# Performance work log

Hardware: AMD Instinct MI355X
Metric: run time of the kernel (lower is better)

The kernel has to match this reference:

```python
import jax, jax.numpy as jnp
from jax import lax
import numpy as np

B, T, D, H, N_MID = 1024, 256, 64, 128, 1000000

def setup_inputs() -> dict:
    key = jax.random.key(0)
    ks = jax.random.split(key, 7)
    item_his = jax.random.randint(ks[0], (B, T), 0, N_MID)
    seq_lens = jax.random.randint(ks[1], (B,), 0, T)
    embedding = jax.random.normal(ks[2], (N_MID, D), dtype=jnp.float32) * 0.05
    gate_kernel = jax.random.normal(ks[3], (D + H, 2 * H), dtype=jnp.float32) * 0.05
    gate_bias = jax.random.normal(ks[4], (2 * H,), dtype=jnp.float32) * 0.05
    cand_kernel = jax.random.normal(ks[5], (D + H, H), dtype=jnp.float32) * 0.05
    cand_bias = jax.random.normal(ks[6], (H,), dtype=jnp.float32) * 0.05
    return {"item_his": item_his, "seq_lens": seq_lens, "embedding": embedding,
            "gate_kernel": gate_kernel, "gate_bias": gate_bias,
            "cand_kernel": cand_kernel, "cand_bias": cand_bias}

def _gru_final_state(x, seq_lens, gate_kernel, gate_bias, cand_kernel, cand_bias):
    # x: [B, T, D]; TF GRUCell math with dynamic_rnn sequence_length masking.
    b, t, d = x.shape
    h_dim = cand_bias.shape[0]
    mask = jnp.arange(t)[None, :] < seq_lens[:, None]  # [B, T]

    def step(h, inp):
        xt, m = inp  # xt: [B, D], m: [B]
        xh = jnp.concatenate([xt, h], axis=-1)              # [B, D+H]
        g = jax.nn.sigmoid(xh @ gate_kernel + gate_bias)    # [B, 2H]
        r, u = jnp.split(g, 2, axis=-1)
        xrh = jnp.concatenate([xt, r * h], axis=-1)
        c = jnp.tanh(xrh @ cand_kernel + cand_bias)
        h_new = u * h + (1.0 - u) * c
        h = jnp.where(m[:, None], h_new, h)  # copy-through past seq end
        return h, None

    h0 = jnp.zeros((b, h_dim), dtype=x.dtype)
    xs = (jnp.swapaxes(x, 0, 1), jnp.swapaxes(mask, 0, 1))
    hT, _ = lax.scan(step, h0, xs)
    return hT

def reference(item_his, seq_lens, embedding, gate_kernel, gate_bias, cand_kernel, cand_bias):
    x = embedding[item_his]  # [B, T, D]
    user_eb = _gru_final_state(x, seq_lens, gate_kernel, gate_bias, cand_kernel, cand_bias)
    return user_eb
```

## Files before the change

kernel.cpp:

```cpp
#include <hip/hip_runtime.h>


#define T_   256
#define D_   64
#define H_   128
#define SROW 208

typedef _Float16 half8_t  __attribute__((ext_vector_type(8)));
typedef float    floatx4  __attribute__((ext_vector_type(4)));

__global__ __launch_bounds__(512, 2) void gru_mfma(
    const int* __restrict__ item_his,
    const int* __restrict__ seq_lens,
    const float* __restrict__ emb,
    const float* __restrict__ Wg,
    const float* __restrict__ bg,
    const float* __restrict__ Wc,
    const float* __restrict__ bc,
    float* __restrict__ out)
{
    __shared__ __align__(16) _Float16 XA[16][SROW];
    __shared__ __align__(16) _Float16 XC[16][SROW];

    const int tid  = threadIdx.x;
    const int w    = tid >> 6;
    const int lane = tid & 63;
    const int row0 = blockIdx.x * 4;

    const int bq = lane >> 4;
    const int bn = lane & 15;
    half8_t BG0[6], BG1[6], BC6[6];
    #pragma unroll
    for (int kt = 0; kt < 6; ++kt) {
        half8_t f0, f1, fc;
        #pragma unroll
        for (int i = 0; i < 8; ++i) {
            const int k = kt * 32 + bq * 8 + i;
            f0[i] = (_Float16)Wg[k * 256 + (w * 16 + bn)];
            f1[i] = (_Float16)Wg[k * 256 + (128 + w * 16 + bn)];
            fc[i] = (_Float16)Wc[k * 128 + (w * 16 + bn)];
        }
        BG0[kt] = f0; BG1[kt] = f1; BC6[kt] = fc;
    }

    const float bgR = bg[w * 16 + bn];
    const float bgU = bg[128 + w * 16 + bn];
    const float bcC = bc[w * 16 + bn];

    int len[4];
    #pragma unroll
    for (int r = 0; r < 4; ++r) len[r] = seq_lens[row0 + r];
    const int maxlen = max(max(len[0], len[1]), max(len[2], len[3]));

    {
        unsigned* pa = (unsigned*)&XA[0][0];
        unsigned* pc = (unsigned*)&XC[0][0];
        for (int i = tid; i < 16 * SROW / 2; i += 512) { pa[i] = 0u; pc[i] = 0u; }
    }
    __syncthreads();

    const int  row_l = w >> 1;
    const int  d_l   = (w & 1) * 32 + (lane & 31);
    const bool ldr   = (lane < 32);

    float xprev = 0.f;
    if (ldr) {
        const int idx = item_his[(row0 + row_l) * T_ + 0];
        xprev = emb[(size_t)idx * D_ + d_l];
        const _Float16 xh = (_Float16)xprev;
        XA[row_l][d_l] = xh;
        XC[row_l][d_l] = xh;
    }
    float h[4] = {0.f, 0.f, 0.f, 0.f};
    float u[4] = {0.f, 0.f, 0.f, 0.f};
    __syncthreads();

    for (int t = 0; t < maxlen; ++t) {
        if (ldr) XC[row_l][d_l] = (_Float16)xprev;
        float xnew = 0.f;
        if (ldr) {
            const int idx = item_his[(row0 + row_l) * T_ + (t + 1)];
            xnew = emb[(size_t)idx * D_ + d_l];
        }

        floatx4 aR = {0.f, 0.f, 0.f, 0.f};
        floatx4 aU = {0.f, 0.f, 0.f, 0.f};
        #pragma unroll
        for (int kt = 0; kt < 6; ++kt) {
            const half8_t af = *(const half8_t*)&XA[lane & 15][kt * 32 + (lane >> 4) * 8];
            aR = __builtin_amdgcn_mfma_f32_16x16x32_f16(af, BG0[kt], aR, 0, 0, 0);
            aU = __builtin_amdgcn_mfma_f32_16x16x32_f16(af, BG1[kt], aU, 0, 0, 0);
        }
        if (lane < 16) {
            #pragma unroll
            for (int r = 0; r < 4; ++r) {
                const float rg = 1.f / (1.f + __expf(-(aR[r] + bgR)));
                u[r]           = 1.f / (1.f + __expf(-(aU[r] + bgU)));
                XC[r][64 + w * 16 + lane] = (_Float16)(rg * h[r]);
            }
        }
        __syncthreads();

        if (ldr) XA[row_l][d_l] = (_Float16)xnew;

        floatx4 aC = {0.f, 0.f, 0.f, 0.f};
        #pragma unroll
        for (int kt = 0; kt < 6; ++kt) {
            const half8_t af = *(const half8_t*)&XC[lane & 15][kt * 32 + (lane >> 4) * 8];
            aC = __builtin_amdgcn_mfma_f32_16x16x32_f16(af, BC6[kt], aC, 0, 0, 0);
        }
        if (lane < 16) {
            #pragma unroll
            for (int r = 0; r < 4; ++r) {
                float s = aC[r] + bcC;
                s = fminf(fmaxf(s, -15.f), 15.f);
                const float e = __expf(2.f * s);
                const float c = (e - 1.f) / (e + 1.f);
                const float hn = u[r] * h[r] + (1.f - u[r]) * c;
                if (t < len[r]) h[r] = hn;
                XA[r][64 + w * 16 + lane] = (_Float16)h[r];
            }
        }
        xprev = xnew;
        __syncthreads();
    }

    if (lane < 16) {
        #pragma unroll
        for (int r = 0; r < 4; ++r)
            out[(row0 + r) * H_ + w * 16 + lane] = h[r];
    }
}

extern "C" void kernel_launch(void* const* d_in, const int* in_sizes, int n_in,
                              void* d_out, int out_size, void* d_ws, size_t ws_size,
                              hipStream_t stream) {
    const int*   item_his = (const int*)d_in[0];
    const int*   seq_lens = (const int*)d_in[1];
    const float* emb      = (const float*)d_in[2];
    const float* Wg       = (const float*)d_in[3];
    const float* bg       = (const float*)d_in[4];
    const float* Wc       = (const float*)d_in[5];
    const float* bc       = (const float*)d_in[6];
    float*       out      = (float*)d_out;

    gru_mfma<<<256, 512, 0, stream>>>(item_his, seq_lens, emb, Wg, bg, Wc, bc, out);
}
```

Before: 644.9 us.

## Split GRU across 512 blocks of 4 waves, two rows and two column tiles per wave

Each block now handles 2 batch rows with 4 waves instead of 4 rows with 8 waves, and each wave computes two 16-column tiles of the gate and candidate outputs. The goal is to fill more CUs (512 blocks vs 256 on a many-CU GPU) and cut barrier cost with fewer waves per block, while reaching maxlen sooner because the per-block maximum covers only 2 rows. In exchange each wave holds twice as many weight fragments in registers and issues twice as many MFMAs per step, and the 16-row MFMA tiles now carry only 2 useful rows, which wastes more compute.

```diff
diff --git a/kernel.cpp b/kernel.cpp
--- a/kernel.cpp
+++ b/kernel.cpp
@@ -9,7 +9,7 @@
 typedef _Float16 half8_t  __attribute__((ext_vector_type(8)));
 typedef float    floatx4  __attribute__((ext_vector_type(4)));
 
-__global__ __launch_bounds__(512, 2) void gru_mfma(
+__global__ __launch_bounds__(256, 2) void gru_mfma2(
     const int* __restrict__ item_his,
     const int* __restrict__ seq_lens,
     const float* __restrict__ emb,
@@ -25,54 +25,63 @@
     const int tid  = threadIdx.x;
     const int w    = tid >> 6;
     const int lane = tid & 63;
-    const int row0 = blockIdx.x * 4;
+    const int row0 = blockIdx.x * 2;
 
     const int bq = lane >> 4;
     const int bn = lane & 15;
-    half8_t BG0[6], BG1[6], BC6[6];
+    half8_t BR[2][6], BU[2][6], BCf[2][6];
     #pragma unroll
-    for (int kt = 0; kt < 6; ++kt) {
-        half8_t f0, f1, fc;
+    for (int ct = 0; ct < 2; ++ct) {
+        const int colg = (w + 4 * ct) * 16 + bn;
         #pragma unroll
-        for (int i = 0; i < 8; ++i) {
-            const int k = kt * 32 + bq * 8 + i;
-            f0[i] = (_Float16)Wg[k * 256 + (w * 16 + bn)];
-            f1[i] = (_Float16)Wg[k * 256 + (128 + w * 16 + bn)];
-            fc[i] = (_Float16)Wc[k * 128 + (w * 16 + bn)];
+        for (int kt = 0; kt < 6; ++kt) {
+            half8_t fr, fu, fc;
+            #pragma unroll
+            for (int i = 0; i < 8; ++i) {
+                const int k = kt * 32 + bq * 8 + i;
+                fr[i] = (_Float16)Wg[k * 256 + colg];
+                fu[i] = (_Float16)Wg[k * 256 + 128 + colg];
+                fc[i] = (_Float16)Wc[k * 128 + colg];
+            }
+            BR[ct][kt] = fr; BU[ct][kt] = fu; BCf[ct][kt] = fc;
         }
-        BG0[kt] = f0; BG1[kt] = f1; BC6[kt] = fc;
     }
 
-    const float bgR = bg[w * 16 + bn];
-    const float bgU = bg[128 + w * 16 + bn];
-    const float bcC = bc[w * 16 + bn];
+    float bgR[2], bgU[2], bcC[2];
+    #pragma unroll
+    for (int ct = 0; ct < 2; ++ct) {
+        const int colg = (w + 4 * ct) * 16 + bn;
+        bgR[ct] = bg[colg];
+        bgU[ct] = bg[128 + colg];
+        bcC[ct] = bc[colg];
+    }
 
-    int len[4];
-    #pragma unroll
-    for (int r = 0; r < 4; ++r) len[r] = seq_lens[row0 + r];
-    const int maxlen = max(max(len[0], len[1]), max(len[2], len[3]));
+    int len[2];
+    len[0] = seq_lens[row0 + 0];
+    len[1] = seq_lens[row0 + 1];
+    const int maxlen = max(len[0], len[1]);
 
     {
         unsigned* pa = (unsigned*)&XA[0][0];
         unsigned* pc = (unsigned*)&XC[0][0];
-        for (int i = tid; i < 16 * SROW / 2; i += 512) { pa[i] = 0u; pc[i] = 0u; }
+        for (int i = tid; i < 16 * SROW / 2; i += 256) { pa[i] = 0u; pc[i] = 0u; }
     }
     __syncthreads();
 
-    const int  row_l = w >> 1;
-    const int  d_l   = (w & 1) * 32 + (lane & 31);
-    const bool ldr   = (lane < 32);
+    const bool ldr   = (tid < 128);
+    const int  row_l = tid >> 6;
+    const int  d_l   = tid & 63;
 
     float xprev = 0.f;
-    if (ldr) {
+    if (ldr && maxlen > 0) {
         const int idx = item_his[(row0 + row_l) * T_ + 0];
         xprev = emb[(size_t)idx * D_ + d_l];
         const _Float16 xh = (_Float16)xprev;
         XA[row_l][d_l] = xh;
         XC[row_l][d_l] = xh;
     }
-    float h[4] = {0.f, 0.f, 0.f, 0.f};
-    float u[4] = {0.f, 0.f, 0.f, 0.f};
+    float h[2][2] = {{0.f, 0.f}, {0.f, 0.f}};
+    float u[2][2] = {{0.f, 0.f}, {0.f, 0.f}};
     __syncthreads();
 
     for (int t = 0; t < maxlen; ++t) {
@@ -83,42 +92,51 @@
             xnew = emb[(size_t)idx * D_ + d_l];
         }
 
-        floatx4 aR = {0.f, 0.f, 0.f, 0.f};
-        floatx4 aU = {0.f, 0.f, 0.f, 0.f};
+        floatx4 aR[2] = {{0.f,0.f,0.f,0.f},{0.f,0.f,0.f,0.f}};
+        floatx4 aU[2] = {{0.f,0.f,0.f,0.f},{0.f,0.f,0.f,0.f}};
         #pragma unroll
         for (int kt = 0; kt < 6; ++kt) {
-            const half8_t af = *(const half8_t*)&XA[lane & 15][kt * 32 + (lane >> 4) * 8];
-            aR = __builtin_amdgcn_mfma_f32_16x16x32_f16(af, BG0[kt], aR, 0, 0, 0);
-            aU = __builtin_amdgcn_mfma_f32_16x16x32_f16(af, BG1[kt], aU, 0, 0, 0);
+            const half8_t af = *(const half8_t*)&XA[bn][kt * 32 + bq * 8];
+            aR[0] = __builtin_amdgcn_mfma_f32_16x16x32_f16(af, BR[0][kt], aR[0], 0, 0, 0);
+            aU[0] = __builtin_amdgcn_mfma_f32_16x16x32_f16(af, BU[0][kt], aU[0], 0, 0, 0);
+            aR[1] = __builtin_amdgcn_mfma_f32_16x16x32_f16(af, BR[1][kt], aR[1], 0, 0, 0);
+            aU[1] = __builtin_amdgcn_mfma_f32_16x16x32_f16(af, BU[1][kt], aU[1], 0, 0, 0);
         }
         if (lane < 16) {
             #pragma unroll
-            for (int r = 0; r < 4; ++r) {
-                const float rg = 1.f / (1.f + __expf(-(aR[r] + bgR)));
-                u[r]           = 1.f / (1.f + __expf(-(aU[r] + bgU)));
-                XC[r][64 + w * 16 + lane] = (_Float16)(rg * h[r]);
+            for (int ct = 0; ct < 2; ++ct) {
+                #pragma unroll
+                for (int r = 0; r < 2; ++r) {
+                    const float rg = 1.f / (1.f + __expf(-(aR[ct][r] + bgR[ct])));
+                    u[r][ct]       = 1.f / (1.f + __expf(-(aU[ct][r] + bgU[ct])));
+                    XC[r][64 + (w + 4 * ct) * 16 + lane] = (_Float16)(rg * h[r][ct]);
+                }
             }
         }
         __syncthreads();
 
         if (ldr) XA[row_l][d_l] = (_Float16)xnew;
 
-        floatx4 aC = {0.f, 0.f, 0.f, 0.f};
+        floatx4 aC[2] = {{0.f,0.f,0.f,0.f},{0.f,0.f,0.f,0.f}};
         #pragma unroll
         for (int kt = 0; kt < 6; ++kt) {
-            const half8_t af = *(const half8_t*)&XC[lane & 15][kt * 32 + (lane >> 4) * 8];
-            aC = __builtin_amdgcn_mfma_f32_16x16x32_f16(af, BC6[kt], aC, 0, 0, 0);
+            const half8_t af = *(const half8_t*)&XC[bn][kt * 32 + bq * 8];
+            aC[0] = __builtin_amdgcn_mfma_f32_16x16x32_f16(af, BCf[0][kt], aC[0], 0, 0, 0);
+            aC[1] = __builtin_amdgcn_mfma_f32_16x16x32_f16(af, BCf[1][kt], aC[1], 0, 0, 0);
         }
         if (lane < 16) {
             #pragma unroll
-            for (int r = 0; r < 4; ++r) {
-                float s = aC[r] + bcC;
-                s = fminf(fmaxf(s, -15.f), 15.f);
-                const float e = __expf(2.f * s);
-                const float c = (e - 1.f) / (e + 1.f);
-                const float hn = u[r] * h[r] + (1.f - u[r]) * c;
-                if (t < len[r]) h[r] = hn;
-                XA[r][64 + w * 16 + lane] = (_Float16)h[r];
+            for (int ct = 0; ct < 2; ++ct) {
+                #pragma unroll
+                for (int r = 0; r < 2; ++r) {
+                    float s = aC[ct][r] + bcC[ct];
+                    s = fminf(fmaxf(s, -15.f), 15.f);
+                    const float e = __expf(2.f * s);
+                    const float c = (e - 1.f) / (e + 1.f);
+                    const float hn = u[r][ct] * h[r][ct] + (1.f - u[r][ct]) * c;
+                    if (t < len[r]) h[r][ct] = hn;
+                    XA[r][64 + (w + 4 * ct) * 16 + lane] = (_Float16)h[r][ct];
+                }
             }
         }
         xprev = xnew;
@@ -127,8 +145,10 @@
 
     if (lane < 16) {
         #pragma unroll
-        for (int r = 0; r < 4; ++r)
-            out[(row0 + r) * H_ + w * 16 + lane] = h[r];
+        for (int ct = 0; ct < 2; ++ct)
+            #pragma unroll
+            for (int r = 0; r < 2; ++r)
+                out[(row0 + r) * H_ + (w + 4 * ct) * 16 + lane] = h[r][ct];
     }
 }
 
@@ -144,5 +164,5 @@
     const float* bc       = (const float*)d_in[6];
     float*       out      = (float*)d_out;
 
-    gru_mfma<<<256, 512, 0, stream>>>(item_his, seq_lens, emb, Wg, bg, Wc, bc, out);
+    gru_mfma2<<<512, 256, 0, stream>>>(item_his, seq_lens, emb, Wg, bg, Wc, bc, out);
 }
```

New measurement: 698.8 us. 8.4% more time.
